# Optimization experiments

Measured on AMD Instinct MI355X. Metric: run time of the kernel, lower is better.

Reference implementation:

```python
import jax, jax.numpy as jnp
import numpy as np

ALPHA = 0.1       # args.alpha
T = 1.0           # args.T temperature
SIGMA = 64.0      # Gaussian kernel bandwidth of kernel_function
B_CONST = 1.0     # B in get_lambda
N_ITERS = 50      # 2^-50 << tol=1e-8, matches the break condition of the 1000-iter loop
HW = 256          # image resolution (upsample target)


def _features(feat):
    # get_feature: bilinear upsample (align_corners=False == half-pixel, as jax.image.resize) then sigmoid(x/T)
    n, c, _, _ = feat.shape
    up = jax.image.resize(feat, (n, c, HW, HW), method='bilinear')
    return jax.nn.sigmoid(up / T)


def setup_inputs() -> dict:
    key = jax.random.key(0)
    k1, k2, k3, k4 = jax.random.split(key, 4)
    return {
        'cal_feat': jax.random.normal(k1, (256, 1, 64, 64), jnp.float32),
        'test_feat': jax.random.normal(k2, (32, 1, 64, 64), jnp.float32),
        'cal_gt': jax.random.randint(k3, (256, 1, 256, 256), 0, 2, jnp.int32),
        'test_gt': jax.random.randint(k4, (32, 1, 256, 256), 0, 2, jnp.int32),
    }


def reference(cal_feat, test_feat, cal_gt, test_gt):
    cal_res = _features(cal_feat)    # [N,1,H,W] in (0,1)
    test_res = _features(test_feat)  # [B,1,H,W]
    N = cal_res.shape[0]
    B = test_res.shape[0]
    f32 = cal_res.dtype

    # kernel_function.get_weight: Gaussian RBF on flattened features, plus self-weight 1, row-normalized -> [B, N+1]
    cf = cal_res.reshape(N, -1)
    tf = test_res.reshape(B, -1)
    d2 = (tf * tf).sum(-1)[:, None] + (cf * cf).sum(-1)[None, :] - 2.0 * (tf @ cf.T)
    k = jnp.exp(-d2 / (2.0 * SIGMA * SIGMA))
    w = jnp.concatenate([k, jnp.ones((B, 1), f32)], axis=1)
    w = w / w.sum(axis=1, keepdims=True)

    # FNR_i(t) = #{positive pixels of cal sample i with score < t} / #positives
    # (pred = res >= t, so false negatives are positive pixels with res < t). Precompute sorted
    # positive-pixel scores per cal sample so the bisection is a batched searchsorted.
    gt = (cal_gt > 0).reshape(N, -1)
    pos = jnp.sum(gt, axis=1)                                    # [N]
    scores = jnp.where(gt, cal_res.reshape(N, -1), jnp.inf)
    sorted_scores = jnp.sort(scores, axis=1)                     # [N, HW*HW], padding at +inf
    pos_f = jnp.maximum(pos, 1).astype(f32)

    def fnr_at(t):  # t: [B] thresholds -> [N, B]
        cnt = jax.vmap(lambda s: jnp.searchsorted(s, t, side='left'))(sorted_scores)
        return cnt.astype(f32) / pos_f[:, None]

    # batched bisection on lambda (get_lambda, vectorized over the B test samples)
    def body(carry, _):
        low, high = carry
        lam = 0.5 * (low + high)
        fnr = fnr_at(1.0 - lam)                                   # [N, B]
        risk = jnp.einsum('bn,nb->b', w[:, :-1], fnr) + w[:, -1] * B_CONST
        high = jnp.where(risk < ALPHA, lam, high)
        low = jnp.where(risk >= ALPHA, lam, low)
        return (low, high), None

    init = (jnp.zeros((B,), f32), jnp.ones((B,), f32))
    (low, _), _ = jax.lax.scan(body, init, None, length=N_ITERS)
    lam = low  # _lambda = low after the loop

    # prediction set, size and per-test FNR (get_fnr_list on the test sample)
    pred = test_res >= (1.0 - lam)[:, None, None, None]           # [B,1,H,W] bool
    size = jnp.sum(pred, axis=(1, 2, 3)).astype(f32)
    tgt = test_gt > 0
    tp = jnp.sum(pred & tgt, axis=(1, 2, 3)).astype(f32)
    tpos = jnp.maximum(jnp.sum(tgt, axis=(1, 2, 3)), 1).astype(f32)
    fnr_test = 1.0 - tp / tpos                                    # fdr_tensor, [B]
    return fnr_test, lam, size
```

## Files before the change

kernel.cpp:

```cpp
#include <hip/hip_runtime.h>


#define NPIX 65536
#define HB 16256
#define CDF_STRIDE 16272
#define ALPHA 0.1f
#define STAGE_CAP 35840

#define OFF_TESTRES  0
#define OFF_CALBF    8388608u
#define OFF_TESTBF   41943040u
#define OFF_GROUPED  46137344u
#define OFF_CDF      79691776u
#define OFF_GPART    96354304u
#define OFF_CC       98451456u
#define OFF_THR      98452480u
#define OFF_LAM      98452608u
#define OFF_FACC     98452736u

typedef __attribute__((ext_vector_type(8))) short bf16x8;
typedef __attribute__((ext_vector_type(16))) float f32x16;

__device__ __forceinline__ unsigned short f2bf_rne(float f) {
  unsigned u = __float_as_uint(f);
  return (unsigned short)((u + 0x7FFFu + ((u >> 16) & 1u)) >> 16);
}

__device__ __forceinline__ int SW(int w) { return w ^ ((w >> 5) & 31); }

__device__ __forceinline__ float score_at(const float* __restrict__ sfeat,
                                          int x0, int x1, float wx, int y) {
  float sy = 0.25f * (float)y - 0.375f;
  int y0 = (int)floorf(sy);
  float wy = sy - (float)y0;
  int y1 = y0 + 1;
  if (y0 < 0) y0 = 0;
  if (y1 > 63) y1 = 63;
  float a = sfeat[y0 * 64 + x0] * (1.f - wx) + sfeat[y0 * 64 + x1] * wx;
  float b = sfeat[y1 * 64 + x0] * (1.f - wx) + sfeat[y1 * 64 + x1] * wx;
  float v = a * (1.f - wy) + b * wy;
  return 1.f / (1.f + __expf(-v));
}

__global__ __launch_bounds__(1024, 2) void k_calt(const float* __restrict__ featc,
                                                  const int* __restrict__ gt,
                                                  unsigned short* __restrict__ calbf,
                                                  unsigned* __restrict__ cdf,
                                                  unsigned short* __restrict__ grouped,
                                                  float* __restrict__ cc,
                                                  const float* __restrict__ featt,
                                                  float* __restrict__ tres,
                                                  unsigned short* __restrict__ tbf) {
  __shared__ unsigned smem[17313];
  __shared__ float sfeat[4096];
  __shared__ __align__(16) unsigned short sstage[STAGE_CAP];
  float* tfeat = (float*)sstage;
  const int tid = threadIdx.x;
  const int lane = tid & 63, wv = tid >> 6;
  const int x = tid & 255, yq = tid >> 8;
  float sx = 0.25f * (float)x - 0.375f;
  int x0 = (int)floorf(sx);
  float wx = sx - (float)x0;
  int x1 = x0 + 1;
  if (x0 < 0) x0 = 0;
  if (x1 > 63) x1 = 63;

  const int n = blockIdx.x;
  const int b = n >> 3, sl = n & 7;
  for (int i = tid; i < HB; i += 1024) smem[i] = 0;
  for (int i = tid; i < 4096; i += 1024) {
    sfeat[i] = featc[n * 4096 + i];
    tfeat[i] = featt[b * 4096 + i];
  }
  const int* gtn = gt + (size_t)n * NPIX;
  unsigned short* cbn = calbf + (size_t)n * NPIX;
  __syncthreads();

  {
    float* resb = tres + (size_t)b * NPIX + sl * 8192;
    unsigned short* tbn = tbf + (size_t)b * NPIX + sl * 8192;
    #pragma unroll
    for (int i = 0; i < 8; ++i) {
      int y = sl * 32 + i * 4 + yq;
      float s = score_at(tfeat, x0, x1, wx, y);
      int q = i * 1024 + tid;
      resb[q] = s;
      tbn[q] = f2bf_rne(s);
    }
  }

  unsigned long long pm = 0ull;
  float sumsq = 0.f;
  #pragma unroll 8
  for (int it = 0; it < 64; ++it) {
    int y = it * 4 + yq;
    float s = score_at(sfeat, x0, x1, wx, y);
    int p = (y << 8) + x;
    unsigned short bh = f2bf_rne(s);
    cbn[p] = bh;
    float sr = __uint_as_float((unsigned)bh << 16);
    sumsq += sr * sr;
    if (gtn[p] > 0) {
      pm |= (1ull << it);
      atomicAdd(&smem[SW((int)(__float_as_uint(s) >> 16))], 1u);
    }
  }
  #pragma unroll
  for (int off = 32; off; off >>= 1) sumsq += __shfl_xor(sumsq, off);
  if (lane == 0) smem[16272 + wv] = __float_as_uint(sumsq);
  __syncthreads();
  if (tid == 0) {
    float c = 0.f;
    for (int w = 0; w < 16; ++w) c += __uint_as_float(smem[16272 + w]);
    cc[n] = c;
  }
  const int base = tid * 16;
  unsigned psum = 0;
  if (tid < 1016) {
    #pragma unroll
    for (int j = 0; j < 16; ++j) psum += smem[SW(base + j)];
  }
  unsigned inc = psum;
  #pragma unroll
  for (int off = 1; off < 64; off <<= 1) {
    unsigned v = __shfl_up(inc, off);
    if (lane >= off) inc += v;
  }
  if (lane == 63) smem[16256 + wv] = inc;
  smem[16288 + tid] = inc - psum;
  __syncthreads();
  {
    unsigned woff = 0;
    for (int w = 0; w < wv; ++w) woff += smem[16256 + w];
    unsigned run = woff + smem[16288 + tid];
    if (tid < 1016) {
      #pragma unroll
      for (int j = 0; j < 16; ++j) {
        int si = SW(base + j);
        unsigned h = smem[si];
        smem[si] = run;
        run += h;
      }
    }
    if (tid == 1015) smem[17312] = run;
  }
  __syncthreads();
  unsigned* cdfn = cdf + (size_t)n * CDF_STRIDE;
  for (int i = tid; i < HB; i += 1024) cdfn[i] = smem[SW(i)];
  const unsigned pos = smem[17312];
  if (tid == 0) cdfn[HB] = pos;
  __syncthreads();
  unsigned short* gn = grouped + (size_t)n * NPIX;
  for (int it = 0; it < 64; ++it) {
    if (pm & (1ull << it)) {
      int y = it * 4 + yq;
      float s = score_at(sfeat, x0, x1, wx, y);
      unsigned bits = __float_as_uint(s);
      unsigned idx = atomicAdd(&smem[SW((int)(bits >> 16))], 1u);
      unsigned short lo = (unsigned short)(bits & 0xFFFFu);
      if (idx < STAGE_CAP) sstage[idx] = lo;
      else gn[idx] = lo;
    }
  }
  __syncthreads();
  unsigned lim = pos < STAGE_CAP ? pos : STAGE_CAP;
  for (unsigned i = tid; i < lim; i += 1024) gn[i] = sstage[i];
}

__global__ __launch_bounds__(256) void k_gemm(const unsigned short* __restrict__ tbf,
                                              const unsigned short* __restrict__ cbf,
                                              float* __restrict__ gpart) {
  __shared__ __align__(16) unsigned short As[16384];
  __shared__ __align__(16) unsigned short Bs[16384];
  __shared__ float lred[4][1024];
  const int tid = threadIdx.x;
  const int lane = tid & 63, wv = tid >> 6;
  const int r = lane & 31, half = lane >> 5;
  const int nt = blockIdx.x;
  f32x16 acc;
  #pragma unroll
  for (int i = 0; i < 16; ++i) acc[i] = 0.f;
  for (int ch = 0; ch < 2; ++ch) {
    const size_t kbase = (size_t)blockIdx.y * 1024 + ch * 512;
    __syncthreads();
    #pragma unroll
    for (int s = 0; s < 16; ++s) {
      int flat = s * 256 + tid;
      int rem = flat & 2047;
      int row = rem >> 6, kb = rem & 63;
      const unsigned short* src = (flat >= 2048)
          ? cbf + (size_t)(nt * 32 + row) * NPIX + kbase + kb * 8
          : tbf + (size_t)row * NPIX + kbase + kb * 8;
      int slot = ((kb << 5) + row) ^ (kb & 31);
      int4 v = *(const int4*)src;
      *(int4*)((flat >= 2048 ? Bs : As) + slot * 8) = v;
    }
    __syncthreads();
    #pragma unroll
    for (int i = 0; i < 8; ++i) {
      int k8 = (wv << 4) + i * 2 + half;
      int slot = ((k8 << 5) + r) ^ (k8 & 31);
      bf16x8 a = *(const bf16x8*)(As + slot * 8);
      bf16x8 b = *(const bf16x8*)(Bs + slot * 8);
      acc = __builtin_amdgcn_mfma_f32_32x32x16_bf16(a, b, acc, 0, 0, 0);
    }
  }
  #pragma unroll
  for (int rg = 0; rg < 16; ++rg) {
    int m = (rg & 3) + 8 * (rg >> 2) + 4 * half;
    lred[wv][m * 32 + r] = acc[rg];
  }
  __syncthreads();
  float* gp = gpart + (size_t)(blockIdx.y * 8 + nt) * 1024;
  for (int e = tid; e < 1024; e += 256)
    gp[e] = lred[0][e] + lred[1][e] + lred[2][e] + lred[3][e];
}

__global__ __launch_bounds__(512) void k_quantw(const float* __restrict__ gpart,
                                                const float* __restrict__ cc,
                                                const unsigned short* __restrict__ tbf,
                                                const unsigned* __restrict__ cdf,
                                                const unsigned short* __restrict__ grouped,
                                                float* __restrict__ lam,
                                                float* __restrict__ thr,
                                                int* __restrict__ facc) {
  __shared__ float qs[256];
  __shared__ float bins[4096];
  __shared__ float red[8];
  __shared__ float tpart[16];
  __shared__ float bc[3];
  __shared__ unsigned sBin;
  const int b = blockIdx.x, tid = threadIdx.x;
  const int lane = tid & 63, wv = tid >> 6;

  if (tid < 4) facc[b * 4 + tid] = 0;
  for (int i = tid; i < 4096; i += 512) bins[i] = 0.f;
  if (tid == 0) sBin = 0xFFFFFFFFu;

  {
    const unsigned short* tbn = tbf + (size_t)b * NPIX;
    const int xa = tid & 255, ya = tid >> 8;
    const int yb = ya + 2;
    float sa = 0.f, sb = 0.f;
    #pragma unroll 4
    for (int it = 0; it < 64; ++it) {
      float ra = __uint_as_float((unsigned)tbn[((it * 4 + ya) << 8) + xa] << 16);
      float rb = __uint_as_float((unsigned)tbn[((it * 4 + yb) << 8) + xa] << 16);
      sa += ra * ra;
      sb += rb * rb;
    }
    #pragma unroll
    for (int off = 32; off; off >>= 1) {
      sa += __shfl_xor(sa, off);
      sb += __shfl_xor(sb, off);
    }
    if (lane == 0) { tpart[wv] = sa; tpart[8 + wv] = sb; }
  }
  __syncthreads();
  if (tid == 0) {
    float t = 0.f;
    for (int w = 0; w < 16; ++w) t += tpart[w];
    bc[2] = t;
  }
  float g = 0.f;
  if (tid < 256) {
    const float* gp = gpart + ((tid >> 5) * 1024) + (b * 32) + (tid & 31);
    #pragma unroll 8
    for (int ks = 0; ks < 64; ++ks) g += gp[(size_t)ks * 8192];
  }
  __syncthreads();
  float k = 0.f;
  if (tid < 256) {
    float d2 = bc[2] + cc[tid] - 2.f * g;
    k = expf(-d2 * (1.f / 8192.f));
  }
  float v = k;
  #pragma unroll
  for (int off = 32; off; off >>= 1) v += __shfl_xor(v, off);
  if (lane == 0) red[wv] = v;
  __syncthreads();
  if (tid == 0) {
    float ws = 1.f;
    for (int w = 0; w < 8; ++w) ws += red[w];
    bc[0] = ws;
  }
  __syncthreads();
  const float wsum = bc[0];
  const float wlast = 1.f / wsum;
  const float R = ALPHA - wlast;
  if (R <= 0.f) {
    if (tid == 0) { lam[b] = 1.0f; thr[b] = 0.0f; }
    return;
  }
  if (tid < 256) {
    unsigned pos = cdf[(size_t)tid * CDF_STRIDE + HB];
    qs[tid] = k / (wsum * (float)(pos ? pos : 1u));
  }
  __syncthreads();

  int lo = 0, hi = HB;
  float baseS = 0.f;
  for (int it = 0; it < 14; ++it) {
    int mid = (lo + hi) >> 1;
    float p = 0.f;
    if (tid < 256) p = qs[tid] * (float)cdf[(size_t)tid * CDF_STRIDE + mid];
    float r = p;
    #pragma unroll
    for (int off = 32; off; off >>= 1) r += __shfl_xor(r, off);
    if (lane == 0) red[wv] = r;
    __syncthreads();
    if (tid == 0) {
      float s = 0.f;
      for (int w = 0; w < 8; ++w) s += red[w];
      bc[1] = s;
    }
    __syncthreads();
    float S = bc[1];
    if (S < R) { lo = mid; baseS = S; } else { hi = mid; }
  }
  const int B = lo;

  {
    const int n = tid >> 1;
    const float q = qs[n];
    const unsigned* cn = cdf + (size_t)n * CDF_STRIDE;
    const unsigned short* gn = grouped + (size_t)n * NPIX;
    unsigned e0 = cn[B + 1];
    for (unsigned j = cn[B] + (tid & 1); j < e0; j += 2)
      atomicAdd(&bins[gn[j] >> 4], q);
  }
  __syncthreads();

  if (wv == 0) {
    float s = 0.f;
    for (int j = 0; j < 64; ++j) s += bins[lane * 64 + j];
    float inc = s;
    #pragma unroll
    for (int off = 1; off < 64; off <<= 1) {
      float u = __shfl_up(inc, off);
      if (lane >= off) inc += u;
    }
    float pre = inc - s;
    bool hit = (baseS + pre < R) && (baseS + inc >= R);
    unsigned long long m = __ballot(hit);
    int ow = m ? (__ffsll((unsigned long long)m) - 1) : -1;
    if (lane == ow) {
      float run = baseS + pre;
      unsigned bin = (unsigned)lane * 64 + 63;
      for (int j = 0; j < 64; ++j) {
        float bv = bins[lane * 64 + j];
        if (run + bv >= R) { bin = (unsigned)lane * 64 + j; break; }
        run += bv;
      }
      sBin = bin;
    }
    if (m == 0 && lane == 0) sBin = 4095u;
  }
  __syncthreads();
  if (tid == 0) {
    unsigned tb = ((unsigned)B << 16) | (sBin << 4);
    lam[b] = 1.0f - __uint_as_float(tb | 0x8u);
    thr[b] = __uint_as_float((tb | 0xFu) + 1u);
  }
}

__global__ __launch_bounds__(256) void k_finalp(const float* __restrict__ tres,
                                                const int* __restrict__ tgt,
                                                const float* __restrict__ thr,
                                                int* __restrict__ facc) {
  __shared__ int red[12];
  const int b = blockIdx.x, seg = blockIdx.y, tid = threadIdx.x;
  const int lane = tid & 63, wv = tid >> 6;
  const float th = thr[b];
  const float4* rb4 = (const float4*)(tres + (size_t)b * NPIX + seg * 8192);
  const int4* gb4 = (const int4*)(tgt + (size_t)b * NPIX + seg * 8192);
  int sz = 0, tp = 0, tpos = 0;
  #pragma unroll
  for (int i = 0; i < 8; ++i) {
    float4 r4 = rb4[i * 256 + tid];
    int4 g4 = gb4[i * 256 + tid];
    int p0 = (r4.x >= th), t0 = (g4.x > 0);
    int p1 = (r4.y >= th), t1 = (g4.y > 0);
    int p2 = (r4.z >= th), t2 = (g4.z > 0);
    int p3 = (r4.w >= th), t3 = (g4.w > 0);
    sz += p0 + p1 + p2 + p3;
    tp += (p0 & t0) + (p1 & t1) + (p2 & t2) + (p3 & t3);
    tpos += t0 + t1 + t2 + t3;
  }
  #pragma unroll
  for (int off = 32; off; off >>= 1) {
    sz += __shfl_xor(sz, off);
    tp += __shfl_xor(tp, off);
    tpos += __shfl_xor(tpos, off);
  }
  if (lane == 0) { red[wv] = sz; red[4 + wv] = tp; red[8 + wv] = tpos; }
  __syncthreads();
  if (tid == 0) {
    int s0 = red[0] + red[1] + red[2] + red[3];
    int s1 = red[4] + red[5] + red[6] + red[7];
    int s2 = red[8] + red[9] + red[10] + red[11];
    atomicAdd(&facc[b * 4 + 0], s0);
    atomicAdd(&facc[b * 4 + 1], s1);
    atomicAdd(&facc[b * 4 + 2], s2);
  }
}

__global__ void k_out(const int* __restrict__ facc, const float* __restrict__ lam,
                      float* __restrict__ out) {
  int b = threadIdx.x;
  if (b < 32) {
    int sz = facc[b * 4], tp = facc[b * 4 + 1], tpos = facc[b * 4 + 2];
    float tposf = (float)(tpos > 0 ? tpos : 1);
    out[b] = 1.f - (float)tp / tposf;
    out[32 + b] = lam[b];
    out[64 + b] = (float)sz;
  }
}

extern "C" void kernel_launch(void* const* d_in, const int* in_sizes, int n_in,
                              void* d_out, int out_size, void* d_ws, size_t ws_size,
                              hipStream_t stream) {
  const float* cal_feat = (const float*)d_in[0];
  const float* test_feat = (const float*)d_in[1];
  const int* cal_gt = (const int*)d_in[2];
  const int* test_gt = (const int*)d_in[3];
  float* out = (float*)d_out;
  char* ws = (char*)d_ws;

  float* test_res = (float*)(ws + OFF_TESTRES);
  unsigned short* cal_bf = (unsigned short*)(ws + OFF_CALBF);
  unsigned short* test_bf = (unsigned short*)(ws + OFF_TESTBF);
  unsigned short* grouped = (unsigned short*)(ws + OFF_GROUPED);
  unsigned* cdf = (unsigned*)(ws + OFF_CDF);
  float* gpart = (float*)(ws + OFF_GPART);
  float* cc = (float*)(ws + OFF_CC);
  float* thr = (float*)(ws + OFF_THR);
  float* lam = (float*)(ws + OFF_LAM);
  int* facc = (int*)(ws + OFF_FACC);

  k_calt<<<dim3(256), dim3(1024), 0, stream>>>(cal_feat, cal_gt, cal_bf, cdf, grouped, cc,
                                               test_feat, test_res, test_bf);
  k_gemm<<<dim3(8, 64), dim3(256), 0, stream>>>(test_bf, cal_bf, gpart);
  k_quantw<<<dim3(32), dim3(512), 0, stream>>>(gpart, cc, test_bf, cdf, grouped,
                                               lam, thr, facc);
  k_finalp<<<dim3(32, 8), dim3(256), 0, stream>>>(test_res, test_gt, thr, facc);
  k_out<<<dim3(1), dim3(64), 0, stream>>>(facc, lam, out);
}
```

Baseline: 242.7 us.

## Reuse horizontal interpolants across rows, narrow CDF to 16-bit, fuse output kernel

The cal-score loop is reorganised so each thread walks 16 contiguous source rows and reuses the horizontally interpolated values between consecutive output rows. This cuts shared-memory reads per pixel, and the test-image loop gets the same change. The per-sample CDF array is stored as 16-bit instead of 32-bit to halve its write and read traffic, which assumes positive counts never exceed 65535; with 65536 pixels an all-positive sample would overflow. The final output kernel is folded into k_finalp using a last-block-done atomic counter, which removes one launch.

After: 239.7 us. Within noise of the previous version (-1.2%).

```diff
diff --git a/kernel.cpp b/kernel.cpp
--- a/kernel.cpp
+++ b/kernel.cpp
@@ -12,11 +12,11 @@
 #define OFF_TESTBF   41943040u
 #define OFF_GROUPED  46137344u
 #define OFF_CDF      79691776u
-#define OFF_GPART    96354304u
-#define OFF_CC       98451456u
-#define OFF_THR      98452480u
-#define OFF_LAM      98452608u
-#define OFF_FACC     98452736u
+#define OFF_GPART    88023040u
+#define OFF_CC       90120192u
+#define OFF_THR      90121216u
+#define OFF_LAM      90121344u
+#define OFF_FACC     90121472u
 
 typedef __attribute__((ext_vector_type(8))) short bf16x8;
 typedef __attribute__((ext_vector_type(16))) float f32x16;
@@ -28,16 +28,7 @@
 
 __device__ __forceinline__ int SW(int w) { return w ^ ((w >> 5) & 31); }
 
-__device__ __forceinline__ float score_at(const float* __restrict__ sfeat,
-                                          int x0, int x1, float wx, int y) {
-  float sy = 0.25f * (float)y - 0.375f;
-  int y0 = (int)floorf(sy);
-  float wy = sy - (float)y0;
-  int y1 = y0 + 1;
-  if (y0 < 0) y0 = 0;
-  if (y1 > 63) y1 = 63;
-  float a = sfeat[y0 * 64 + x0] * (1.f - wx) + sfeat[y0 * 64 + x1] * wx;
-  float b = sfeat[y1 * 64 + x0] * (1.f - wx) + sfeat[y1 * 64 + x1] * wx;
+__device__ __forceinline__ float sig_v(float a, float b, float wy) {
   float v = a * (1.f - wy) + b * wy;
   return 1.f / (1.f + __expf(-v));
 }
@@ -45,7 +36,7 @@
 __global__ __launch_bounds__(1024, 2) void k_calt(const float* __restrict__ featc,
                                                   const int* __restrict__ gt,
                                                   unsigned short* __restrict__ calbf,
-                                                  unsigned* __restrict__ cdf,
+                                                  unsigned short* __restrict__ cdf,
                                                   unsigned short* __restrict__ grouped,
                                                   float* __restrict__ cc,
                                                   const float* __restrict__ featt,
@@ -77,32 +68,66 @@
   __syncthreads();
 
   {
-    float* resb = tres + (size_t)b * NPIX + sl * 8192;
-    unsigned short* tbn = tbf + (size_t)b * NPIX + sl * 8192;
-    #pragma unroll
-    for (int i = 0; i < 8; ++i) {
-      int y = sl * 32 + i * 4 + yq;
-      float s = score_at(tfeat, x0, x1, wx, y);
-      int q = i * 1024 + tid;
-      resb[q] = s;
-      tbn[q] = f2bf_rne(s);
-    }
-  }
-
+    const float* tf0 = tfeat + x0;
+    const float* tf1 = tfeat + x1;
+    float* resb = tres + (size_t)b * NPIX;
+    unsigned short* tbn = tbf + (size_t)b * NPIX;
+    const int mt0 = sl * 8 + yq * 2;
+    int rp = mt0 - 1 < 0 ? 0 : mt0 - 1;
+    float hp = tf0[rp * 64] * (1.f - wx) + tf1[rp * 64] * wx;
+    float hc = tf0[mt0 * 64] * (1.f - wx) + tf1[mt0 * 64] * wx;
+    #pragma unroll
+    for (int q = 0; q < 2; ++q) {
+      int m = mt0 + q;
+      int rn = m + 1 > 63 ? 63 : m + 1;
+      float hn = tf0[rn * 64] * (1.f - wx) + tf1[rn * 64] * wx;
+      #pragma unroll
+      for (int j = 0; j < 4; ++j) {
+        int y = 4 * m + j;
+        float sy = 0.25f * (float)y - 0.375f;
+        int y0 = (int)floorf(sy);
+        float wy = sy - (float)y0;
+        float s = sig_v(j < 2 ? hp : hc, j < 2 ? hc : hn, wy);
+        int p = (y << 8) + x;
+        resb[p] = s;
+        tbn[p] = f2bf_rne(s);
+      }
+      hp = hc; hc = hn;
+    }
+  }
+
+  const float* f0 = sfeat + x0;
+  const float* f1 = sfeat + x1;
+  const int m0 = yq * 16;
   unsigned long long pm = 0ull;
   float sumsq = 0.f;
-  #pragma unroll 8
-  for (int it = 0; it < 64; ++it) {
-    int y = it * 4 + yq;
-    float s = score_at(sfeat, x0, x1, wx, y);
-    int p = (y << 8) + x;
-    unsigned short bh = f2bf_rne(s);
-    cbn[p] = bh;
-    float sr = __uint_as_float((unsigned)bh << 16);
-    sumsq += sr * sr;
-    if (gtn[p] > 0) {
-      pm |= (1ull << it);
-      atomicAdd(&smem[SW((int)(__float_as_uint(s) >> 16))], 1u);
+  {
+    int rp = m0 - 1 < 0 ? 0 : m0 - 1;
+    float hp = f0[rp * 64] * (1.f - wx) + f1[rp * 64] * wx;
+    float hc = f0[m0 * 64] * (1.f - wx) + f1[m0 * 64] * wx;
+    #pragma unroll 4
+    for (int q = 0; q < 16; ++q) {
+      int m = m0 + q;
+      int rn = m + 1 > 63 ? 63 : m + 1;
+      float hn = f0[rn * 64] * (1.f - wx) + f1[rn * 64] * wx;
+      #pragma unroll
+      for (int j = 0; j < 4; ++j) {
+        int y = 4 * m + j;
+        float sy = 0.25f * (float)y - 0.375f;
+        int y0 = (int)floorf(sy);
+        float wy = sy - (float)y0;
+        float s = sig_v(j < 2 ? hp : hc, j < 2 ? hc : hn, wy);
+        int p = (y << 8) + x;
+        unsigned short bh = f2bf_rne(s);
+        cbn[p] = bh;
+        float sr = __uint_as_float((unsigned)bh << 16);
+        sumsq += sr * sr;
+        if (gtn[p] > 0) {
+          pm |= (1ull << (q * 4 + j));
+          atomicAdd(&smem[SW((int)(__float_as_uint(s) >> 16))], 1u);
+        }
+      }
+      hp = hc; hc = hn;
     }
   }
   #pragma unroll
@@ -145,21 +170,39 @@
     if (tid == 1015) smem[17312] = run;
   }
   __syncthreads();
-  unsigned* cdfn = cdf + (size_t)n * CDF_STRIDE;
-  for (int i = tid; i < HB; i += 1024) cdfn[i] = smem[SW(i)];
+  unsigned short* cdfn = cdf + (size_t)n * CDF_STRIDE;
+  for (int i = tid; i < HB; i += 1024) cdfn[i] = (unsigned short)smem[SW(i)];
   const unsigned pos = smem[17312];
-  if (tid == 0) cdfn[HB] = pos;
+  if (tid == 0) cdfn[HB] = (unsigned short)pos;
   __syncthreads();
   unsigned short* gn = grouped + (size_t)n * NPIX;
-  for (int it = 0; it < 64; ++it) {
-    if (pm & (1ull << it)) {
-      int y = it * 4 + yq;
-      float s = score_at(sfeat, x0, x1, wx, y);
-      unsigned bits = __float_as_uint(s);
-      unsigned idx = atomicAdd(&smem[SW((int)(bits >> 16))], 1u);
-      unsigned short lo = (unsigned short)(bits & 0xFFFFu);
-      if (idx < STAGE_CAP) sstage[idx] = lo;
-      else gn[idx] = lo;
+  {
+    int rp = m0 - 1 < 0 ? 0 : m0 - 1;
+    float hp = f0[rp * 64] * (1.f - wx) + f1[rp * 64] * wx;
+    float hc = f0[m0 * 64] * (1.f - wx) + f1[m0 * 64] * wx;
+    for (int q = 0; q < 16; ++q) {
+      int m = m0 + q;
+      int rn = m + 1 > 63 ? 63 : m + 1;
+      float hn = f0[rn * 64] * (1.f - wx) + f1[rn * 64] * wx;
+      unsigned nib = (unsigned)(pm >> (q * 4)) & 0xFu;
+      if (nib) {
+        #pragma unroll
+        for (int j = 0; j < 4; ++j) {
+          if (nib & (1u << j)) {
+            int y = 4 * m + j;
+            float sy = 0.25f * (float)y - 0.375f;
+            int y0 = (int)floorf(sy);
+            float wy = sy - (float)y0;
+            float s = sig_v(j < 2 ? hp : hc, j < 2 ? hc : hn, wy);
+            unsigned bits = __float_as_uint(s);
+            unsigned idx = atomicAdd(&smem[SW((int)(bits >> 16))], 1u);
+            unsigned short lo = (unsigned short)(bits & 0xFFFFu);
+            if (idx < STAGE_CAP) sstage[idx] = lo;
+            else gn[idx] = lo;
+          }
+        }
+      }
+      hp = hc; hc = hn;
     }
   }
   __syncthreads();
@@ -219,7 +262,7 @@
 __global__ __launch_bounds__(512) void k_quantw(const float* __restrict__ gpart,
                                                 const float* __restrict__ cc,
                                                 const unsigned short* __restrict__ tbf,
-                                                const unsigned* __restrict__ cdf,
+                                                const unsigned short* __restrict__ cdf,
                                                 const unsigned short* __restrict__ grouped,
                                                 float* __restrict__ lam,
                                                 float* __restrict__ thr,
@@ -323,10 +366,10 @@
   {
     const int n = tid >> 1;
     const float q = qs[n];
-    const unsigned* cn = cdf + (size_t)n * CDF_STRIDE;
+    const unsigned short* cn = cdf + (size_t)n * CDF_STRIDE;
     const unsigned short* gn = grouped + (size_t)n * NPIX;
     unsigned e0 = cn[B + 1];
-    for (unsigned j = cn[B] + (tid & 1); j < e0; j += 2)
+    for (unsigned j = (unsigned)cn[B] + (tid & 1); j < e0; j += 2)
       atomicAdd(&bins[gn[j] >> 4], q);
   }
   __syncthreads();
@@ -367,7 +410,9 @@
 __global__ __launch_bounds__(256) void k_finalp(const float* __restrict__ tres,
                                                 const int* __restrict__ tgt,
                                                 const float* __restrict__ thr,
-                                                int* __restrict__ facc) {
+                                                const float* __restrict__ lam,
+                                                int* __restrict__ facc,
+                                                float* __restrict__ out) {
   __shared__ int red[12];
   const int b = blockIdx.x, seg = blockIdx.y, tid = threadIdx.x;
   const int lane = tid & 63, wv = tid >> 6;
@@ -402,18 +447,17 @@
     atomicAdd(&facc[b * 4 + 0], s0);
     atomicAdd(&facc[b * 4 + 1], s1);
     atomicAdd(&facc[b * 4 + 2], s2);
-  }
-}
-
-__global__ void k_out(const int* __restrict__ facc, const float* __restrict__ lam,
-                      float* __restrict__ out) {
-  int b = threadIdx.x;
-  if (b < 32) {
-    int sz = facc[b * 4], tp = facc[b * 4 + 1], tpos = facc[b * 4 + 2];
-    float tposf = (float)(tpos > 0 ? tpos : 1);
-    out[b] = 1.f - (float)tp / tposf;
-    out[32 + b] = lam[b];
-    out[64 + b] = (float)sz;
+    __threadfence();
+    int done = atomicAdd(&facc[b * 4 + 3], 1);
+    if (done == 7) {
+      int f0 = atomicAdd(&facc[b * 4 + 0], 0);
+      int f1 = atomicAdd(&facc[b * 4 + 1], 0);
+      int f2 = atomicAdd(&facc[b * 4 + 2], 0);
+      float tposf = (float)(f2 > 0 ? f2 : 1);
+      out[b] = 1.f - (float)f1 / tposf;
+      out[32 + b] = lam[b];
+      out[64 + b] = (float)f0;
+    }
   }
 }
 
@@ -431,7 +475,7 @@
   unsigned short* cal_bf = (unsigned short*)(ws + OFF_CALBF);
   unsigned short* test_bf = (unsigned short*)(ws + OFF_TESTBF);
   unsigned short* grouped = (unsigned short*)(ws + OFF_GROUPED);
-  unsigned* cdf = (unsigned*)(ws + OFF_CDF);
+  unsigned short* cdf = (unsigned short*)(ws + OFF_CDF);
   float* gpart = (float*)(ws + OFF_GPART);
   float* cc = (float*)(ws + OFF_CC);
   float* thr = (float*)(ws + OFF_THR);
@@ -443,6 +487,5 @@
   k_gemm<<<dim3(8, 64), dim3(256), 0, stream>>>(test_bf, cal_bf, gpart);
   k_quantw<<<dim3(32), dim3(512), 0, stream>>>(gpart, cc, test_bf, cdf, grouped,
                                                lam, thr, facc);
-  k_finalp<<<dim3(32, 8), dim3(256), 0, stream>>>(test_res, test_gt, thr, facc);
-  k_out<<<dim3(1), dim3(64), 0, stream>>>(facc, lam, out);
-}
+  k_finalp<<<dim3(32, 8), dim3(256), 0, stream>>>(test_res, test_gt, thr, lam, facc, out);
+}
```
